# Optimization experiments

Measured on AMD Instinct MI355X. Metric: run time of the kernel, lower is better.

## Reference

```python
import jax, jax.numpy as jnp
import numpy as np

N = 50000        # nodes
E = 800000       # edges (avg degree 16)
IN = 128         # in_feats
HF = 128         # h_feats
HID = (IN + HF) // 2  # 128, per math.floor((h_feats+in_feats)/2)


def setup_inputs() -> dict:
    key = jax.random.key(0)
    ks = jax.random.split(key, 13)

    def glorot(k, fan_in, fan_out):
        s = (2.0 / (fan_in + fan_out)) ** 0.5
        return jax.random.normal(k, (fan_in, fan_out), jnp.float32) * s

    dims = [(IN, HID), (HID, HID), (HID, HID), (HID, HID), (HID, HF)]
    inp = {
        "in_feat": jax.random.normal(ks[0], (N, IN), jnp.float32),
        "src": jax.random.randint(ks[1], (E,), 0, N),
        "dst": jax.random.randint(ks[2], (E,), 0, N),
    }
    for i, (a, b) in enumerate(dims):
        inp[f"W{i+1}"] = glorot(ks[3 + i], a, b)
        inp[f"b{i+1}"] = jnp.zeros((b,), jnp.float32)
    return inp


def reference(in_feat, src, dst, W1, W2, W3, W4, W5, b1, b2, b3, b4, b5):
    # DGL GraphConv, norm='both': y = D_in^{-1/2} * A^T * (D_out^{-1/2} * x) @ W + b
    ones = jnp.ones((src.shape[0],), in_feat.dtype)
    deg_out = jnp.clip(jax.ops.segment_sum(ones, src, num_segments=N), 1.0)
    deg_in = jnp.clip(jax.ops.segment_sum(ones, dst, num_segments=N), 1.0)
    ns = (deg_out ** -0.5)[:, None]  # source-side norm [N,1]
    nd = (deg_in ** -0.5)[:, None]   # dest-side norm   [N,1]

    def conv(x, W, b):
        m = jax.ops.segment_sum((x * ns)[src], dst, num_segments=N)  # [N,D]
        return (m * nd) @ W + b

    h = in_feat
    for W, b in ((W1, b1), (W2, b2), (W3, b3), (W4, b4), (W5, b5)):
        h = jax.nn.relu(conv(h, W, b))

    # vectorized version of the per-element Python double loop threshold
    h_clone = jnp.where(h >= 0.5, jnp.float32(1.0), jnp.float32(0.0))
    return h, h_clone
```

## Files before the change

kernel.cpp:

```cpp
#include <hip/hip_runtime.h>

#define FEAT 128
#define RANGE 12800
#define NSLICE 64

typedef _Float16 half8 __attribute__((ext_vector_type(8)));
typedef _Float16 half4v __attribute__((ext_vector_type(4)));
typedef float f32x4 __attribute__((ext_vector_type(4)));

__global__ __launch_bounds__(1024) void hist_kernel(const int* __restrict__ src,
                                                    const int* __restrict__ dst,
                                                    unsigned* __restrict__ partialD,
                                                    unsigned* __restrict__ partialS,
                                                    int E, int NP) {
    __shared__ unsigned hpk[RANGE / 2];
    int per = (NP / RANGE) * NSLICE;
    int b = blockIdx.x;
    int halfsel = b / per;
    int q = b % per;
    int r = q / NSLICE;
    int s = q % NSLICE;
    const int* arr = halfsel ? src : dst;
    unsigned* out = halfsel ? partialS : partialD;
    int v0 = r * RANGE;
    int tid = threadIdx.x;
    for (int i = tid; i < RANGE / 2; i += 1024) hpk[i] = 0;
    __syncthreads();
    int e0 = (int)((long long)E * s / NSLICE);
    int e1 = (int)((long long)E * (s + 1) / NSLICE);
    for (int e = e0 + tid; e < e1; e += 1024) {
        unsigned d = (unsigned)(arr[e] - v0);
        if (d < RANGE) atomicAdd(&hpk[d >> 1], (d & 1) ? 65536u : 1u);
    }
    __syncthreads();
    size_t wbase = ((size_t)s * NP + v0) >> 1;
    for (int i = tid; i < RANGE / 2; i += 1024) out[wbase + i] = hpk[i];
}

__global__ __launch_bounds__(256) void scanp1_kernel(const unsigned short* __restrict__ pD,
                                                     const unsigned short* __restrict__ pS,
                                                     int* __restrict__ blockSums,
                                                     float* __restrict__ ns,
                                                     float* __restrict__ nd,
                                                     int NP, int n) {
    __shared__ int buf[256];
    int tid = threadIdx.x;
    int v = blockIdx.x * 256 + tid;
    int ssum = 0, osum = 0;
    #pragma unroll
    for (int s = 0; s < NSLICE; ++s) {
        ssum += pD[(size_t)s * NP + v];
        osum += pS[(size_t)s * NP + v];
    }
    if (v < n) {
        ns[v] = 1.0f / sqrtf((float)(osum < 1 ? 1 : osum));
        nd[v] = 1.0f / sqrtf((float)(ssum < 1 ? 1 : ssum));
    }
    buf[tid] = ssum;
    __syncthreads();
    #pragma unroll
    for (int off = 1; off < 256; off <<= 1) {
        int t = (tid >= off) ? buf[tid - off] : 0;
        __syncthreads();
        buf[tid] += t;
        __syncthreads();
    }
    if (tid == 255) blockSums[blockIdx.x] = buf[255];
}

__global__ __launch_bounds__(256) void scanp2_kernel(const int* __restrict__ blockSums,
                                                     int* __restrict__ blockOffs, int nb) {
    __shared__ int buf[256];
    int tid = threadIdx.x;
    int v = (tid < nb) ? blockSums[tid] : 0;
    buf[tid] = v;
    __syncthreads();
    #pragma unroll
    for (int off = 1; off < 256; off <<= 1) {
        int t = (tid >= off) ? buf[tid - off] : 0;
        __syncthreads();
        buf[tid] += t;
        __syncthreads();
    }
    if (tid < nb) blockOffs[tid] = buf[tid] - v;
}

__global__ __launch_bounds__(256) void scanp3_kernel(const unsigned short* __restrict__ pD,
                                                     const int* __restrict__ blockOffs,
                                                     int* __restrict__ cursorV,
                                                     int* __restrict__ offsc,
                                                     int NP, int n) {
    __shared__ int buf[256];
    int tid = threadIdx.x;
    int v = blockIdx.x * 256 + tid;
    int ssum = 0;
    #pragma unroll
    for (int s = 0; s < NSLICE; ++s) ssum += pD[(size_t)s * NP + v];
    buf[tid] = ssum;
    __syncthreads();
    #pragma unroll
    for (int off = 1; off < 256; off <<= 1) {
        int t = (tid >= off) ? buf[tid - off] : 0;
        __syncthreads();
        buf[tid] += t;
        __syncthreads();
    }
    int o = blockOffs[blockIdx.x] + buf[tid] - ssum;
    if (v <= n) offsc[v] = o;
    int* cv = cursorV + (size_t)v * NSLICE;
    #pragma unroll
    for (int s = 0; s < NSLICE; ++s) {
        int val = pD[(size_t)s * NP + v];
        cv[s] = o;
        o += val;
    }
}

__global__ __launch_bounds__(1024) void fill_kernel(const int* __restrict__ src,
                                                    const int* __restrict__ dst,
                                                    const int* __restrict__ cursorV,
                                                    int* __restrict__ esrc, int E, int NP) {
    __shared__ int cur[RANGE];
    int b = blockIdx.x;
    int r = b / NSLICE;
    int inner = b % NSLICE;
    int s = ((inner & 7) << 3) | (inner >> 3);
    int v0 = r * RANGE;
    int tid = threadIdx.x;
    for (int i = tid; i < RANGE; i += 1024)
        cur[i] = cursorV[(size_t)(v0 + i) * NSLICE + s];
    __syncthreads();
    int e0 = (int)((long long)E * s / NSLICE);
    int e1 = (int)((long long)E * (s + 1) / NSLICE);
    for (int e = e0 + tid; e < e1; e += 1024) {
        unsigned dd = (unsigned)(dst[e] - v0);
        if (dd < RANGE) {
            int p = atomicAdd(&cur[dd], 1);
            esrc[p] = src[e];
        }
    }
}

__global__ void prescale_kernel(const float* __restrict__ x, const float* __restrict__ ns,
                                _Float16* __restrict__ xh, int n) {
    int i = blockIdx.x * blockDim.x + threadIdx.x;
    if (i >= n * (FEAT / 8)) return;
    int v = i >> 4;
    float w = ns[v];
    float4 t0 = ((const float4*)x)[i * 2];
    float4 t1 = ((const float4*)x)[i * 2 + 1];
    half8 h;
    h[0] = (_Float16)(t0.x * w); h[1] = (_Float16)(t0.y * w);
    h[2] = (_Float16)(t0.z * w); h[3] = (_Float16)(t0.w * w);
    h[4] = (_Float16)(t1.x * w); h[5] = (_Float16)(t1.y * w);
    h[6] = (_Float16)(t1.z * w); h[7] = (_Float16)(t1.w * w);
    ((float4*)xh)[i] = __builtin_bit_cast(float4, h);
}

__global__ __launch_bounds__(256) void wprep_kernel(const float* __restrict__ Wa,
                                                    const float* __restrict__ Wb,
                                                    const float* __restrict__ Wc,
                                                    const float* __restrict__ Wd,
                                                    const float* __restrict__ We,
                                                    _Float16* __restrict__ w16t,
                                                    _Float16* __restrict__ wrt) {
    int gid = blockIdx.x * 256 + threadIdx.x;
    int l = gid >> 14;
    int idx = gid & 16383;
    int col = idx >> 7;
    int k = idx & 127;
    const float* Wp = (l == 0) ? Wa : (l == 1) ? Wb : (l == 2) ? Wc : (l == 3) ? Wd : We;
    float w = Wp[k * FEAT + col];
    _Float16 h = (_Float16)w;
    _Float16 r = (_Float16)(w - (float)h);
    w16t[gid] = h;
    wrt[gid] = r;
}

__global__ __launch_bounds__(256) void agg_kernel(const _Float16* __restrict__ x,
                                                  const int* __restrict__ offs,
                                                  const int* __restrict__ esrc,
                                                  const float* __restrict__ nd,
                                                  float* __restrict__ m, int n) {
    int gid = blockIdx.x * blockDim.x + threadIdx.x;
    int v = gid >> 6;
    if (v >= n) return;
    int lane = threadIdx.x & 63;
    int q = lane >> 4;
    int c = lane & 15;
    int s0 = offs[v], s1 = offs[v + 1];
    float a0[8] = {0,0,0,0,0,0,0,0};
    float a1[8] = {0,0,0,0,0,0,0,0};
    float a2[8] = {0,0,0,0,0,0,0,0};
    float a3[8] = {0,0,0,0,0,0,0,0};
    int j = s0 + q;
    for (; j + 12 < s1; j += 16) {
        int e0 = esrc[j], e1 = esrc[j + 4], e2 = esrc[j + 8], e3 = esrc[j + 12];
        float4 r0 = ((const float4*)(x + (size_t)e0 * FEAT))[c];
        float4 r1 = ((const float4*)(x + (size_t)e1 * FEAT))[c];
        float4 r2 = ((const float4*)(x + (size_t)e2 * FEAT))[c];
        float4 r3 = ((const float4*)(x + (size_t)e3 * FEAT))[c];
        half8 h0 = __builtin_bit_cast(half8, r0);
        half8 h1 = __builtin_bit_cast(half8, r1);
        half8 h2 = __builtin_bit_cast(half8, r2);
        half8 h3 = __builtin_bit_cast(half8, r3);
        #pragma unroll
        for (int k = 0; k < 8; ++k) {
            a0[k] += (float)h0[k];
            a1[k] += (float)h1[k];
            a2[k] += (float)h2[k];
            a3[k] += (float)h3[k];
        }
    }
    for (; j < s1; j += 4) {
        int e0 = esrc[j];
        float4 r0 = ((const float4*)(x + (size_t)e0 * FEAT))[c];
        half8 h0 = __builtin_bit_cast(half8, r0);
        #pragma unroll
        for (int k = 0; k < 8; ++k) a0[k] += (float)h0[k];
    }
    float r[8];
    #pragma unroll
    for (int k = 0; k < 8; ++k) r[k] = (a0[k] + a1[k]) + (a2[k] + a3[k]);
    #pragma unroll
    for (int k = 0; k < 8; ++k) {
        r[k] += __shfl_xor(r[k], 16);
        r[k] += __shfl_xor(r[k], 32);
    }
    if (lane < 16) {
        float sc = nd[v];
        float4 o0, o1;
        o0.x = r[0] * sc; o0.y = r[1] * sc; o0.z = r[2] * sc; o0.w = r[3] * sc;
        o1.x = r[4] * sc; o1.y = r[5] * sc; o1.z = r[6] * sc; o1.w = r[7] * sc;
        ((float4*)(m + (size_t)v * FEAT))[c * 2] = o0;
        ((float4*)(m + (size_t)v * FEAT))[c * 2 + 1] = o1;
    }
}

template<int MODE>
__global__ __launch_bounds__(256) void gemm_kernel(const float* __restrict__ M,
                                                   const _Float16* __restrict__ w16t,
                                                   const _Float16* __restrict__ wrt,
                                                   const float* __restrict__ bias,
                                                   const float* __restrict__ nsv,
                                                   _Float16* __restrict__ outh,
                                                   float* __restrict__ outf,
                                                   float* __restrict__ out2, int n) {
    __shared__ _Float16 A16s[32 * 128];
    __shared__ _Float16 Ars[32 * 128];
    __shared__ _Float16 W16s[128 * 128];
    __shared__ _Float16 Wrs[128 * 128];
    int tid = threadIdx.x;
    int r0 = blockIdx.x * 32;

    #pragma unroll
    for (int j = 0; j < 8; ++j) {
        int i = tid + j * 256;
        int col = i >> 4, ch = i & 15;
        int d = col * 16 + (ch ^ (col & 7));
        ((float4*)W16s)[d] = ((const float4*)w16t)[i];
        ((float4*)Wrs)[d]  = ((const float4*)wrt)[i];
    }
    #pragma unroll
    for (int j = 0; j < 4; ++j) {
        int i = tid + j * 256;
        int row = i >> 5, c4 = i & 31;
        int gr = r0 + row;
        float4 v = make_float4(0.f, 0.f, 0.f, 0.f);
        if (gr < n) v = ((const float4*)(M + (size_t)gr * FEAT))[c4];
        half4v h, rr;
        h[0] = (_Float16)v.x; h[1] = (_Float16)v.y; h[2] = (_Float16)v.z; h[3] = (_Float16)v.w;
        rr[0] = (_Float16)(v.x - (float)h[0]); rr[1] = (_Float16)(v.y - (float)h[1]);
        rr[2] = (_Float16)(v.z - (float)h[2]); rr[3] = (_Float16)(v.w - (float)h[3]);
        int d = row * 128 + (((c4 >> 1) ^ (row & 7)) << 3) + ((c4 & 1) << 2);
        *(half4v*)(A16s + d) = h;
        *(half4v*)(Ars + d) = rr;
    }
    __syncthreads();

    int lane = tid & 63;
    int w = tid >> 6;
    int l15 = lane & 15;
    int q = lane >> 4;
    int rbase = (w & 1) * 16 + l15;
    int cbase = (w >> 1) * 64;

    f32x4 acc[4] = {{0.f,0.f,0.f,0.f},{0.f,0.f,0.f,0.f},{0.f,0.f,0.f,0.f},{0.f,0.f,0.f,0.f}};
    #pragma unroll
    for (int ks = 0; ks < 4; ++ks) {
        int chunk = ks * 4 + q;
        int aoff = rbase * 128 + ((chunk ^ (rbase & 7)) << 3);
        half8 a16 = *(const half8*)(A16s + aoff);
        half8 ar  = *(const half8*)(Ars + aoff);
        #pragma unroll
        for (int ct = 0; ct < 4; ++ct) {
            int col = cbase + ct * 16 + l15;
            int boff = col * 128 + ((chunk ^ (col & 7)) << 3);
            half8 b16 = *(const half8*)(W16s + boff);
            half8 br  = *(const half8*)(Wrs + boff);
            acc[ct] = __builtin_amdgcn_mfma_f32_16x16x32_f16(a16, b16, acc[ct], 0, 0, 0);
            acc[ct] = __builtin_amdgcn_mfma_f32_16x16x32_f16(a16, br,  acc[ct], 0, 0, 0);
            acc[ct] = __builtin_amdgcn_mfma_f32_16x16x32_f16(ar,  b16, acc[ct], 0, 0, 0);
        }
    }

    int rloc = (w & 1) * 16 + q * 4;
    float scv[4];
    #pragma unroll
    for (int reg = 0; reg < 4; ++reg) {
        int row = r0 + rloc + reg;
        scv[reg] = (MODE == 0 && row < n) ? nsv[row] : 1.0f;
    }
    #pragma unroll
    for (int ct = 0; ct < 4; ++ct) {
        int col = cbase + ct * 16 + l15;
        float b = bias[col];
        #pragma unroll
        for (int reg = 0; reg < 4; ++reg) {
            int row = r0 + rloc + reg;
            if (row < n) {
                float h = acc[ct][reg] + b;
                h = h > 0.f ? h : 0.f;
                if (MODE == 0) {
                    outh[(size_t)row * FEAT + col] = (_Float16)(h * scv[reg]);
                } else {
                    outf[(size_t)row * FEAT + col] = h;
                    out2[(size_t)row * FEAT + col] = h >= 0.5f ? 1.f : 0.f;
                }
            }
        }
    }
}

extern "C" void kernel_launch(void* const* d_in, const int* in_sizes, int n_in,
                              void* d_out, int out_size, void* d_ws, size_t ws_size,
                              hipStream_t stream) {
    const float* in_feat = (const float*)d_in[0];
    const int*   src     = (const int*)d_in[1];
    const int*   dst     = (const int*)d_in[2];
    const float* W[5] = {(const float*)d_in[3], (const float*)d_in[5], (const float*)d_in[7],
                         (const float*)d_in[9], (const float*)d_in[11]};
    const float* B[5] = {(const float*)d_in[4], (const float*)d_in[6], (const float*)d_in[8],
                         (const float*)d_in[10], (const float*)d_in[12]};
    const int E = in_sizes[1];
    const int N = in_sizes[0] / FEAT;
    const int NRANGE = (N + RANGE - 1) / RANGE;
    const int NP = NRANGE * RANGE;
    const size_t MTOT = (size_t)NP * NSLICE;

    char* ws = (char*)d_ws;
    size_t off = 0;
    auto alloc = [&](size_t bytes) { size_t o = off; off += (bytes + 255) & ~size_t(255); return o; };
    unsigned* partialD = (unsigned*)(ws + alloc(MTOT * 2));
    size_t    pS_off   = alloc(MTOT * 2);
    unsigned* partialS = (unsigned*)(ws + pS_off);
    int*      esrc     = (int*)(ws + pS_off);
    size_t    cV_off   = alloc(MTOT * 4);
    int*      cursorV  = (int*)(ws + cV_off);
    _Float16* xh       = (_Float16*)(ws + cV_off);
    float*    ns       = (float*)(ws + alloc((size_t)N * 4));
    float*    nd       = (float*)(ws + alloc((size_t)N * 4));
    int*      offsc    = (int*)(ws + alloc((size_t)(N + 1) * 4));
    int*      blockSums = (int*)(ws + alloc(1024));
    int*      blockOffs = (int*)(ws + alloc(1024));
    _Float16* w16t     = (_Float16*)(ws + alloc(5 * 16384 * 2));
    _Float16* wrt      = (_Float16*)(ws + alloc(5 * 16384 * 2));

    float* out_h = (float*)d_out;
    float* out_c = out_h + (size_t)N * FEAT;

    const int histBlocks = 2 * NRANGE * NSLICE;
    const int scanBlocks = NP / 256;
    hist_kernel<<<histBlocks, 1024, 0, stream>>>(src, dst, partialD, partialS, E, NP);
    scanp1_kernel<<<scanBlocks, 256, 0, stream>>>((const unsigned short*)partialD,
                                                  (const unsigned short*)partialS,
                                                  blockSums, ns, nd, NP, N);
    scanp2_kernel<<<1, 256, 0, stream>>>(blockSums, blockOffs, scanBlocks);
    scanp3_kernel<<<scanBlocks, 256, 0, stream>>>((const unsigned short*)partialD,
                                                  blockOffs, cursorV, offsc, NP, N);
    fill_kernel<<<NRANGE * NSLICE, 1024, 0, stream>>>(src, dst, cursorV, esrc, E, NP);
    wprep_kernel<<<320, 256, 0, stream>>>(W[0], W[1], W[2], W[3], W[4], w16t, wrt);
    prescale_kernel<<<(N * (FEAT / 8) + 255) / 256, 256, 0, stream>>>(in_feat, ns, xh, N);

    const int agg_blocks = (int)(((size_t)N * 64 + 255) / 256);
    const int gemm_blocks = (N + 31) / 32;

    for (int l = 0; l < 5; ++l) {
        agg_kernel<<<agg_blocks, 256, 0, stream>>>(xh, offsc, esrc, nd, out_h, N);
        if (l < 4)
            gemm_kernel<0><<<gemm_blocks, 256, 0, stream>>>(out_h, w16t + (size_t)l * 16384,
                                                            wrt + (size_t)l * 16384, B[l], ns,
                                                            xh, nullptr, nullptr, N);
        else
            gemm_kernel<1><<<gemm_blocks, 256, 0, stream>>>(out_h, w16t + (size_t)l * 16384,
                                                            wrt + (size_t)l * 16384, B[l], nullptr,
                                                            nullptr, out_h, out_c, N);
    }
}
```

Baseline: 465.5 us.

## Replace sliced histogram CSR build with global atomics; retune aggregation and GEMM tiles

Replaces the range/slice shared-memory histogram and per-slice cursor fill with a direct global-atomic degree count, a simple scan, and a global-atomic scatter fill. This removes the large partial-count buffers and the many passes over the edge list. It also maps two edge groups per node instead of four in the aggregation kernel (32 lanes per node), and doubles the GEMM row tile to 64 with 512 threads. The cost is heavy global atomic contention and non-deterministic edge order within each CSR row, plus larger shared memory per GEMM block.

```diff
diff --git a/kernel.cpp b/kernel.cpp
--- a/kernel.cpp
+++ b/kernel.cpp
@@ -1,62 +1,42 @@
 #include <hip/hip_runtime.h>
 
 #define FEAT 128
-#define RANGE 12800
-#define NSLICE 64
 
 typedef _Float16 half8 __attribute__((ext_vector_type(8)));
 typedef _Float16 half4v __attribute__((ext_vector_type(4)));
 typedef float f32x4 __attribute__((ext_vector_type(4)));
 
-__global__ __launch_bounds__(1024) void hist_kernel(const int* __restrict__ src,
-                                                    const int* __restrict__ dst,
-                                                    unsigned* __restrict__ partialD,
-                                                    unsigned* __restrict__ partialS,
-                                                    int E, int NP) {
-    __shared__ unsigned hpk[RANGE / 2];
-    int per = (NP / RANGE) * NSLICE;
-    int b = blockIdx.x;
-    int halfsel = b / per;
-    int q = b % per;
-    int r = q / NSLICE;
-    int s = q % NSLICE;
-    const int* arr = halfsel ? src : dst;
-    unsigned* out = halfsel ? partialS : partialD;
-    int v0 = r * RANGE;
-    int tid = threadIdx.x;
-    for (int i = tid; i < RANGE / 2; i += 1024) hpk[i] = 0;
-    __syncthreads();
-    int e0 = (int)((long long)E * s / NSLICE);
-    int e1 = (int)((long long)E * (s + 1) / NSLICE);
-    for (int e = e0 + tid; e < e1; e += 1024) {
-        unsigned d = (unsigned)(arr[e] - v0);
-        if (d < RANGE) atomicAdd(&hpk[d >> 1], (d & 1) ? 65536u : 1u);
-    }
-    __syncthreads();
-    size_t wbase = ((size_t)s * NP + v0) >> 1;
-    for (int i = tid; i < RANGE / 2; i += 1024) out[wbase + i] = hpk[i];
-}
-
-__global__ __launch_bounds__(256) void scanp1_kernel(const unsigned short* __restrict__ pD,
-                                                     const unsigned short* __restrict__ pS,
-                                                     int* __restrict__ blockSums,
-                                                     float* __restrict__ ns,
-                                                     float* __restrict__ nd,
-                                                     int NP, int n) {
+__global__ __launch_bounds__(256) void zero_kernel(int4* __restrict__ p, int cnt4) {
+    int i = blockIdx.x * 256 + threadIdx.x;
+    if (i < cnt4) p[i] = make_int4(0, 0, 0, 0);
+}
+
+__global__ __launch_bounds__(256) void deg_kernel(const int* __restrict__ src,
+                                                  const int* __restrict__ dst,
+                                                  int* __restrict__ degS,
+                                                  int* __restrict__ degD, int E) {
+    int e = blockIdx.x * 256 + threadIdx.x;
+    if (e < E) {
+        atomicAdd(&degS[src[e]], 1);
+        atomicAdd(&degD[dst[e]], 1);
+    }
+}
+
+__global__ __launch_bounds__(256) void scan1_kernel(const int* __restrict__ degD,
+                                                    const int* __restrict__ degS,
+                                                    int* __restrict__ blockSums,
+                                                    float* __restrict__ ns,
+                                                    float* __restrict__ nd, int n) {
     __shared__ int buf[256];
     int tid = threadIdx.x;
     int v = blockIdx.x * 256 + tid;
-    int ssum = 0, osum = 0;
-    #pragma unroll
-    for (int s = 0; s < NSLICE; ++s) {
-        ssum += pD[(size_t)s * NP + v];
-        osum += pS[(size_t)s * NP + v];
-    }
+    int s = degD[v];
     if (v < n) {
-        ns[v] = 1.0f / sqrtf((float)(osum < 1 ? 1 : osum));
-        nd[v] = 1.0f / sqrtf((float)(ssum < 1 ? 1 : ssum));
-    }
-    buf[tid] = ssum;
+        int o = degS[v];
+        ns[v] = 1.0f / sqrtf((float)(o < 1 ? 1 : o));
+        nd[v] = 1.0f / sqrtf((float)(s < 1 ? 1 : s));
+    }
+    buf[tid] = s;
     __syncthreads();
     #pragma unroll
     for (int off = 1; off < 256; off <<= 1) {
@@ -68,8 +48,8 @@
     if (tid == 255) blockSums[blockIdx.x] = buf[255];
 }
 
-__global__ __launch_bounds__(256) void scanp2_kernel(const int* __restrict__ blockSums,
-                                                     int* __restrict__ blockOffs, int nb) {
+__global__ __launch_bounds__(256) void scan2_kernel(const int* __restrict__ blockSums,
+                                                    int* __restrict__ blockOffs, int nb) {
     __shared__ int buf[256];
     int tid = threadIdx.x;
     int v = (tid < nb) ? blockSums[tid] : 0;
@@ -85,18 +65,15 @@
     if (tid < nb) blockOffs[tid] = buf[tid] - v;
 }
 
-__global__ __launch_bounds__(256) void scanp3_kernel(const unsigned short* __restrict__ pD,
-                                                     const int* __restrict__ blockOffs,
-                                                     int* __restrict__ cursorV,
-                                                     int* __restrict__ offsc,
-                                                     int NP, int n) {
+__global__ __launch_bounds__(256) void scan3_kernel(const int* __restrict__ degD,
+                                                    const int* __restrict__ blockOffs,
+                                                    int* __restrict__ offsc,
+                                                    int* __restrict__ gcursor, int n) {
     __shared__ int buf[256];
     int tid = threadIdx.x;
     int v = blockIdx.x * 256 + tid;
-    int ssum = 0;
-    #pragma unroll
-    for (int s = 0; s < NSLICE; ++s) ssum += pD[(size_t)s * NP + v];
-    buf[tid] = ssum;
+    int s = degD[v];
+    buf[tid] = s;
     __syncthreads();
     #pragma unroll
     for (int off = 1; off < 256; off <<= 1) {
@@ -105,39 +82,19 @@
         buf[tid] += t;
         __syncthreads();
     }
-    int o = blockOffs[blockIdx.x] + buf[tid] - ssum;
+    int o = blockOffs[blockIdx.x] + buf[tid] - s;
     if (v <= n) offsc[v] = o;
-    int* cv = cursorV + (size_t)v * NSLICE;
-    #pragma unroll
-    for (int s = 0; s < NSLICE; ++s) {
-        int val = pD[(size_t)s * NP + v];
-        cv[s] = o;
-        o += val;
-    }
-}
-
-__global__ __launch_bounds__(1024) void fill_kernel(const int* __restrict__ src,
-                                                    const int* __restrict__ dst,
-                                                    const int* __restrict__ cursorV,
-                                                    int* __restrict__ esrc, int E, int NP) {
-    __shared__ int cur[RANGE];
-    int b = blockIdx.x;
-    int r = b / NSLICE;
-    int inner = b % NSLICE;
-    int s = ((inner & 7) << 3) | (inner >> 3);
-    int v0 = r * RANGE;
-    int tid = threadIdx.x;
-    for (int i = tid; i < RANGE; i += 1024)
-        cur[i] = cursorV[(size_t)(v0 + i) * NSLICE + s];
-    __syncthreads();
-    int e0 = (int)((long long)E * s / NSLICE);
-    int e1 = (int)((long long)E * (s + 1) / NSLICE);
-    for (int e = e0 + tid; e < e1; e += 1024) {
-        unsigned dd = (unsigned)(dst[e] - v0);
-        if (dd < RANGE) {
-            int p = atomicAdd(&cur[dd], 1);
-            esrc[p] = src[e];
-        }
+    gcursor[v] = o;
+}
+
+__global__ __launch_bounds__(256) void fill_kernel(const int* __restrict__ src,
+                                                   const int* __restrict__ dst,
+                                                   int* __restrict__ gcursor,
+                                                   int* __restrict__ esrc, int E) {
+    int e = blockIdx.x * 256 + threadIdx.x;
+    if (e < E) {
+        int p = atomicAdd(&gcursor[dst[e]], 1);
+        esrc[p] = src[e];
     }
 }
 
@@ -182,10 +139,10 @@
                                                   const int* __restrict__ esrc,
                                                   const float* __restrict__ nd,
                                                   float* __restrict__ m, int n) {
-    int gid = blockIdx.x * blockDim.x + threadIdx.x;
-    int v = gid >> 6;
+    int gid = blockIdx.x * 256 + threadIdx.x;
+    int v = gid >> 5;
     if (v >= n) return;
-    int lane = threadIdx.x & 63;
+    int lane = threadIdx.x & 31;
     int q = lane >> 4;
     int c = lane & 15;
     int s0 = offs[v], s1 = offs[v + 1];
@@ -194,8 +151,8 @@
     float a2[8] = {0,0,0,0,0,0,0,0};
     float a3[8] = {0,0,0,0,0,0,0,0};
     int j = s0 + q;
-    for (; j + 12 < s1; j += 16) {
-        int e0 = esrc[j], e1 = esrc[j + 4], e2 = esrc[j + 8], e3 = esrc[j + 12];
+    for (; j + 6 < s1; j += 8) {
+        int e0 = esrc[j], e1 = esrc[j + 2], e2 = esrc[j + 4], e3 = esrc[j + 6];
         float4 r0 = ((const float4*)(x + (size_t)e0 * FEAT))[c];
         float4 r1 = ((const float4*)(x + (size_t)e1 * FEAT))[c];
         float4 r2 = ((const float4*)(x + (size_t)e2 * FEAT))[c];
@@ -212,7 +169,7 @@
             a3[k] += (float)h3[k];
         }
     }
-    for (; j < s1; j += 4) {
+    for (; j < s1; j += 2) {
         int e0 = esrc[j];
         float4 r0 = ((const float4*)(x + (size_t)e0 * FEAT))[c];
         half8 h0 = __builtin_bit_cast(half8, r0);
@@ -223,11 +180,8 @@
     #pragma unroll
     for (int k = 0; k < 8; ++k) r[k] = (a0[k] + a1[k]) + (a2[k] + a3[k]);
     #pragma unroll
-    for (int k = 0; k < 8; ++k) {
-        r[k] += __shfl_xor(r[k], 16);
-        r[k] += __shfl_xor(r[k], 32);
-    }
-    if (lane < 16) {
+    for (int k = 0; k < 8; ++k) r[k] += __shfl_xor(r[k], 16);
+    if (q == 0) {
         float sc = nd[v];
         float4 o0, o1;
         o0.x = r[0] * sc; o0.y = r[1] * sc; o0.z = r[2] * sc; o0.w = r[3] * sc;
@@ -238,7 +192,7 @@
 }
 
 template<int MODE>
-__global__ __launch_bounds__(256) void gemm_kernel(const float* __restrict__ M,
+__global__ __launch_bounds__(512) void gemm_kernel(const float* __restrict__ M,
                                                    const _Float16* __restrict__ w16t,
                                                    const _Float16* __restrict__ wrt,
                                                    const float* __restrict__ bias,
@@ -246,16 +200,16 @@
                                                    _Float16* __restrict__ outh,
                                                    float* __restrict__ outf,
                                                    float* __restrict__ out2, int n) {
-    __shared__ _Float16 A16s[32 * 128];
-    __shared__ _Float16 Ars[32 * 128];
+    __shared__ _Float16 A16s[64 * 128];
+    __shared__ _Float16 Ars[64 * 128];
     __shared__ _Float16 W16s[128 * 128];
     __shared__ _Float16 Wrs[128 * 128];
     int tid = threadIdx.x;
-    int r0 = blockIdx.x * 32;
-
-    #pragma unroll
-    for (int j = 0; j < 8; ++j) {
-        int i = tid + j * 256;
+    int r0 = blockIdx.x * 64;
+
+    #pragma unroll
+    for (int j = 0; j < 4; ++j) {
+        int i = tid + j * 512;
         int col = i >> 4, ch = i & 15;
         int d = col * 16 + (ch ^ (col & 7));
         ((float4*)W16s)[d] = ((const float4*)w16t)[i];
@@ -263,7 +217,7 @@
     }
     #pragma unroll
     for (int j = 0; j < 4; ++j) {
-        int i = tid + j * 256;
+        int i = tid + j * 512;
         int row = i >> 5, c4 = i & 31;
         int gr = r0 + row;
         float4 v = make_float4(0.f, 0.f, 0.f, 0.f);
@@ -282,8 +236,9 @@
     int w = tid >> 6;
     int l15 = lane & 15;
     int q = lane >> 4;
-    int rbase = (w & 1) * 16 + l15;
-    int cbase = (w >> 1) * 64;
+    int rw = w & 3, cw = w >> 2;
+    int rbase = rw * 16 + l15;
+    int cbase = cw * 64;
 
     f32x4 acc[4] = {{0.f,0.f,0.f,0.f},{0.f,0.f,0.f,0.f},{0.f,0.f,0.f,0.f},{0.f,0.f,0.f,0.f}};
     #pragma unroll
@@ -304,7 +259,7 @@
         }
     }
 
-    int rloc = (w & 1) * 16 + q * 4;
+    int rloc = rw * 16 + q * 4;
     float scv[4];
     #pragma unroll
     for (int reg = 0; reg < 4; ++reg) {
@@ -344,20 +299,16 @@
                          (const float*)d_in[10], (const float*)d_in[12]};
     const int E = in_sizes[1];
     const int N = in_sizes[0] / FEAT;
-    const int NRANGE = (N + RANGE - 1) / RANGE;
-    const int NP = NRANGE * RANGE;
-    const size_t MTOT = (size_t)NP * NSLICE;
+    const int scanBlocks = (N + 255) / 256;
+    const int NPAD = scanBlocks * 256;
 
     char* ws = (char*)d_ws;
     size_t off = 0;
     auto alloc = [&](size_t bytes) { size_t o = off; off += (bytes + 255) & ~size_t(255); return o; };
-    unsigned* partialD = (unsigned*)(ws + alloc(MTOT * 2));
-    size_t    pS_off   = alloc(MTOT * 2);
-    unsigned* partialS = (unsigned*)(ws + pS_off);
-    int*      esrc     = (int*)(ws + pS_off);
-    size_t    cV_off   = alloc(MTOT * 4);
-    int*      cursorV  = (int*)(ws + cV_off);
-    _Float16* xh       = (_Float16*)(ws + cV_off);
+    int*      degS     = (int*)(ws + alloc((size_t)NPAD * 4));
+    int*      degD     = (int*)(ws + alloc((size_t)NPAD * 4));
+    int*      gcursor  = (int*)(ws + alloc((size_t)NPAD * 4));
+    int*      esrc     = (int*)(ws + alloc((size_t)E * 4));
     float*    ns       = (float*)(ws + alloc((size_t)N * 4));
     float*    nd       = (float*)(ws + alloc((size_t)N * 4));
     int*      offsc    = (int*)(ws + alloc((size_t)(N + 1) * 4));
@@ -365,34 +316,33 @@
     int*      blockOffs = (int*)(ws + alloc(1024));
     _Float16* w16t     = (_Float16*)(ws + alloc(5 * 16384 * 2));
     _Float16* wrt      = (_Float16*)(ws + alloc(5 * 16384 * 2));
+    _Float16* xh       = (_Float16*)(ws + alloc((size_t)N * FEAT * 2));
 
     float* out_h = (float*)d_out;
     float* out_c = out_h + (size_t)N * FEAT;
 
-    const int histBlocks = 2 * NRANGE * NSLICE;
-    const int scanBlocks = NP / 256;
-    hist_kernel<<<histBlocks, 1024, 0, stream>>>(src, dst, partialD, partialS, E, NP);
-    scanp1_kernel<<<scanBlocks, 256, 0, stream>>>((const unsigned short*)partialD,
-                                                  (const unsigned short*)partialS,
-                                                  blockSums, ns, nd, NP, N);
-    scanp2_kernel<<<1, 256, 0, stream>>>(blockSums, blockOffs, scanBlocks);
-    scanp3_kernel<<<scanBlocks, 256, 0, stream>>>((const unsigned short*)partialD,
-                                                  blockOffs, cursorV, offsc, NP, N);
-    fill_kernel<<<NRANGE * NSLICE, 1024, 0, stream>>>(src, dst, cursorV, esrc, E, NP);
+    const int cnt4 = (2 * NPAD) / 4;
+    const int eBlocks = (E + 255) / 256;
+    zero_kernel<<<(cnt4 + 255) / 256, 256, 0, stream>>>((int4*)degS, cnt4);
+    deg_kernel<<<eBlocks, 256, 0, stream>>>(src, dst, degS, degD, E);
+    scan1_kernel<<<scanBlocks, 256, 0, stream>>>(degD, degS, blockSums, ns, nd, N);
+    scan2_kernel<<<1, 256, 0, stream>>>(blockSums, blockOffs, scanBlocks);
+    scan3_kernel<<<scanBlocks, 256, 0, stream>>>(degD, blockOffs, offsc, gcursor, N);
+    fill_kernel<<<eBlocks, 256, 0, stream>>>(src, dst, gcursor, esrc, E);
     wprep_kernel<<<320, 256, 0, stream>>>(W[0], W[1], W[2], W[3], W[4], w16t, wrt);
     prescale_kernel<<<(N * (FEAT / 8) + 255) / 256, 256, 0, stream>>>(in_feat, ns, xh, N);
 
-    const int agg_blocks = (int)(((size_t)N * 64 + 255) / 256);
-    const int gemm_blocks = (N + 31) / 32;
+    const int agg_blocks = (int)(((size_t)N * 32 + 255) / 256);
+    const int gemm_blocks = (N + 63) / 64;
 
     for (int l = 0; l < 5; ++l) {
         agg_kernel<<<agg_blocks, 256, 0, stream>>>(xh, offsc, esrc, nd, out_h, N);
         if (l < 4)
-            gemm_kernel<0><<<gemm_blocks, 256, 0, stream>>>(out_h, w16t + (size_t)l * 16384,
+            gemm_kernel<0><<<gemm_blocks, 512, 0, stream>>>(out_h, w16t + (size_t)l * 16384,
                                                             wrt + (size_t)l * 16384, B[l], ns,
                                                             xh, nullptr, nullptr, N);
         else
-            gemm_kernel<1><<<gemm_blocks, 256, 0, stream>>>(out_h, w16t + (size_t)l * 16384,
+            gemm_kernel<1><<<gemm_blocks, 512, 0, stream>>>(out_h, w16t + (size_t)l * 16384,
                                                             wrt + (size_t)l * 16384, B[l], nullptr,
                                                             nullptr, out_h, out_c, N);
     }
```

Result: slower. 513.3 us (+10.3%).
